# Kernel optimization log

Measured on AMD Instinct MI355X. Metric: run time of the kernel, lower is better.

## Reference

```python
import jax, jax.numpy as jnp
import numpy as np

VOCAB = 50000
EMB = 256
HID = 256
H = HID // 2          # per-direction LSTM hidden
NTAG = 14
START = 12
STOP = 13
SEQ = 8192
NEG = -10000.0


def setup_inputs() -> dict:
    key = jax.random.key(0)
    ks = jax.random.split(key, 14)
    s = 0.1
    sentence = jax.random.randint(ks[0], (SEQ,), 0, VOCAB)
    emb = jax.random.normal(ks[1], (VOCAB, EMB), jnp.float32) * s
    # PyTorch LSTM layout: gates stacked [i, f, g, o], shape [4H, in]
    wih_f = jax.random.normal(ks[2], (4 * H, EMB), jnp.float32) * s
    whh_f = jax.random.normal(ks[3], (4 * H, H), jnp.float32) * s
    bih_f = jax.random.normal(ks[4], (4 * H,), jnp.float32) * s
    bhh_f = jax.random.normal(ks[5], (4 * H,), jnp.float32) * s
    wih_b = jax.random.normal(ks[6], (4 * H, EMB), jnp.float32) * s
    whh_b = jax.random.normal(ks[7], (4 * H, H), jnp.float32) * s
    bih_b = jax.random.normal(ks[8], (4 * H,), jnp.float32) * s
    bhh_b = jax.random.normal(ks[9], (4 * H,), jnp.float32) * s
    w_tag = jax.random.normal(ks[10], (NTAG, HID), jnp.float32) * s
    b_tag = jax.random.normal(ks[11], (NTAG,), jnp.float32) * s
    transitions = jax.random.normal(ks[12], (NTAG, NTAG), jnp.float32)
    transitions = transitions.at[START, :].set(NEG).at[:, STOP].set(NEG)
    return {
        'sentence': sentence, 'emb': emb,
        'wih_f': wih_f, 'whh_f': whh_f, 'bih_f': bih_f, 'bhh_f': bhh_f,
        'wih_b': wih_b, 'whh_b': whh_b, 'bih_b': bih_b, 'bhh_b': bhh_b,
        'w_tag': w_tag, 'b_tag': b_tag, 'transitions': transitions,
    }


def _run_lstm(x, wih, whh, bih, bhh):
    # x: [L, EMB] -> hs: [L, H]; PyTorch gate order i, f, g, o
    def step(carry, xt):
        h, c = carry
        g = xt @ wih.T + h @ whh.T + bih + bhh
        i, f, gg, o = jnp.split(g, 4)
        i = jax.nn.sigmoid(i)
        f = jax.nn.sigmoid(f)
        gg = jnp.tanh(gg)
        o = jax.nn.sigmoid(o)
        c = f * c + i * gg
        h = o * jnp.tanh(c)
        return (h, c), h
    h0 = (jnp.zeros((H,), x.dtype), jnp.zeros((H,), x.dtype))
    _, hs = jax.lax.scan(step, h0, x)
    return hs


def _lstm_feats(sentence, emb, wih_f, whh_f, bih_f, bhh_f,
                wih_b, whh_b, bih_b, bhh_b, w_tag, b_tag):
    x = emb[sentence]                                   # [L, EMB]
    hf = _run_lstm(x, wih_f, whh_f, bih_f, bhh_f)       # [L, H]
    hb = _run_lstm(x[::-1], wih_b, whh_b, bih_b, bhh_b)[::-1]
    out = jnp.concatenate([hf, hb], axis=1)             # [L, HID]
    return out @ w_tag.T + b_tag                        # [L, NTAG]


def _viterbi(feats, transitions):
    init = jnp.full((NTAG,), NEG, feats.dtype).at[START].set(0.0)

    def step(fv, feat):
        scores = fv[None, :] + transitions   # [next_tag, prev_tag]
        bptr = jnp.argmax(scores, axis=1)    # best prev for each next
        fv_new = jnp.max(scores, axis=1) + feat
        return fv_new, bptr

    fv, bptrs = jax.lax.scan(step, init, feats)   # bptrs: [L, NTAG]
    terminal = fv + transitions[STOP]
    best = jnp.argmax(terminal)
    score = terminal[best]

    def back(tag, bptr_t):
        return bptr_t[tag], tag

    # reverse scan: emit tag at each position, walk backpointers to front
    _, path = jax.lax.scan(back, best, bptrs, reverse=True)  # [L]
    return score, path


def reference(sentence, emb, wih_f, whh_f, bih_f, bhh_f,
              wih_b, whh_b, bih_b, bhh_b, w_tag, b_tag, transitions):
    feats = _lstm_feats(sentence, emb, wih_f, whh_f, bih_f, bhh_f,
                        wih_b, whh_b, bih_b, bhh_b, w_tag, b_tag)
    return _viterbi(feats, transitions)
```

## Files before the change

### kernel.cpp

```cpp
#include <hip/hip_runtime.h>
#include <hip/hip_fp16.h>
#include <math.h>

#define SEQ    8192
#define EMBD   256
#define HD     128
#define GATES  512
#define NTAGS  14
#define TAG_START 12
#define TAG_STOP  13
#define NEGV   (-10000.0f)

static constexpr size_t OFF_X     = 0;
static constexpr size_t OFF_WT    = OFF_X + (size_t)SEQ * EMBD;
static constexpr size_t OFF_BSUM  = OFF_WT + (size_t)EMBD * 1024;
static constexpr size_t OFF_GF    = OFF_BSUM + 1024;
static constexpr size_t OFF_GB    = OFF_GF + (size_t)(SEQ + 4) * GATES;
static constexpr size_t OFF_HF    = OFF_GB + (size_t)(SEQ + 4) * GATES;
static constexpr size_t OFF_HB    = OFF_HF + (size_t)SEQ * HD;
static constexpr size_t OFF_FEATS = OFF_HB + (size_t)SEQ * HD;
static constexpr size_t OFF_BP    = OFF_FEATS + (size_t)(SEQ + 8) * 16;
static constexpr size_t OFF_AC    = OFF_BP + (size_t)SEQ * 16 / 4;
static constexpr size_t OFF_FVB   = OFF_AC + (size_t)64 * 256;
static constexpr size_t OFF_SB    = OFF_FVB + 1024;

#define LOG2E  1.4426950408889634f
#define LOG2E2 2.8853900817779268f

typedef _Float16 half2_t __attribute__((ext_vector_type(2)));

__device__ __forceinline__ float fast_rcp(float x) { return __builtin_amdgcn_rcpf(x); }
__device__ __forceinline__ float bcast_lane(float x, int lane) {
  return __int_as_float(__builtin_amdgcn_readlane(__float_as_int(x), lane));
}
__device__ __forceinline__ float max3f(float a, float b, float c) {
  return fmaxf(fmaxf(a, b), c);
}
__device__ __forceinline__ float max14(const float s[NTAGS]) {
  float m0 = max3f(s[0], s[1], s[2]);
  float m1 = max3f(s[3], s[4], s[5]);
  float m2 = max3f(s[6], s[7], s[8]);
  float m3 = max3f(s[9], s[10], s[11]);
  float m4 = fmaxf(s[12], s[13]);
  return max3f(max3f(m0, m1, m2), m3, m4);
}
template<int CTRL>
__device__ __forceinline__ float quad_dpp(float x) {
  int xi = __float_as_int(x);
  int r = __builtin_amdgcn_update_dpp(xi, xi, CTRL, 0xF, 0xF, false);
  return __int_as_float(r);
}

__device__ __forceinline__ float dot2acc(half2_t a, half2_t b, float c) {
#if __has_builtin(__builtin_amdgcn_fdot2)
  return __builtin_amdgcn_fdot2(a, b, c, false);
#else
  return fmaf((float)a[0], (float)b[0], fmaf((float)a[1], (float)b[1], c));
#endif
}

__device__ __forceinline__ float sigf(float x) {
  return fast_rcp(1.0f + exp2f(x * -LOG2E));
}
__device__ __forceinline__ float tanhf_(float x) {
  return fmaf(2.0f, fast_rcp(1.0f + exp2f(x * -LOG2E2)), -1.0f);
}

__device__ __forceinline__ void lds_barrier() {
  __builtin_amdgcn_sched_barrier(0);
  asm volatile("s_waitcnt lgkmcnt(0)" ::: "memory");
  __builtin_amdgcn_s_barrier();
  __builtin_amdgcn_sched_barrier(0);
}

__device__ __forceinline__ void argmax14(const float s[NTAGS], float& bv, int& bi) {
#define MRG(va, ia, vb, ib, vo, io) { bool c_ = (vb) > (va); (vo) = c_ ? (vb) : (va); (io) = c_ ? (ib) : (ia); }
  float v0, v1, v2, v3, v4, v5, v6; int i0, i1, i2, i3, i4, i5, i6;
  MRG(s[0], 0, s[1], 1, v0, i0); MRG(s[2], 2, s[3], 3, v1, i1);
  MRG(s[4], 4, s[5], 5, v2, i2); MRG(s[6], 6, s[7], 7, v3, i3);
  MRG(s[8], 8, s[9], 9, v4, i4); MRG(s[10], 10, s[11], 11, v5, i5);
  MRG(s[12], 12, s[13], 13, v6, i6);
  float w0, w1, w2; int j0, j1, j2;
  MRG(v0, i0, v1, i1, w0, j0); MRG(v2, i2, v3, i3, w1, j1); MRG(v4, i4, v5, i5, w2, j2);
  float x0, x1; int y0, y1;
  MRG(w0, j0, w1, j1, x0, y0); MRG(w2, j2, v6, i6, x1, y1);
  MRG(x0, y0, x1, y1, bv, bi);
#undef MRG
}

__global__ void prep_k(const float* __restrict__ wihf, const float* __restrict__ wihb,
                       const float* __restrict__ bihf, const float* __restrict__ bhhf,
                       const float* __restrict__ bihb, const float* __restrict__ bhhb,
                       float* __restrict__ WT, float* __restrict__ bsum) {
  if (blockIdx.x < 1024) {
    int e = blockIdx.x * 256 + threadIdx.x;
    int k = e >> 10, c = e & 1023;
    int cq = c & 511;
    int src = (cq & 3) * HD + (cq >> 2);
    WT[e] = (c < GATES) ? wihf[(size_t)src * EMBD + k] : wihb[(size_t)src * EMBD + k];
  } else {
    for (int i = 0; i < 4; ++i) {
      int c = threadIdx.x + i * 256;
      int cq = c & 511;
      int src = (cq & 3) * HD + (cq >> 2);
      bsum[c] = (c < GATES) ? (bihf[src] + bhhf[src]) : (bihb[src] + bhhb[src]);
    }
  }
}

__global__ void gather_k(const int* __restrict__ sent, const float* __restrict__ emb,
                         float* __restrict__ X) {
  int t = blockIdx.x;
  int row = sent[t];
  ((float4*)(X + (size_t)t * EMBD))[threadIdx.x] =
      ((const float4*)(emb + (size_t)row * EMBD))[threadIdx.x];
}

__global__ __launch_bounds__(256) void gemm_k(const float* __restrict__ X,
                                              const float* __restrict__ WT,
                                              const float* __restrict__ bsum,
                                              float* __restrict__ Gf, float* __restrict__ Gb) {
  __shared__ __align__(16) float As[32][68];
  __shared__ __align__(16) float Bs[32][64];
  const int tid = threadIdx.x;
  const int cb = blockIdx.x * 64;
  const int tb = blockIdx.y * 64;
  const bool flip = (cb >= GATES);
  const int ty = tid >> 4, tx = tid & 15;
  float acc[4][4] = {};

  const int r  = tid >> 2;
  const int kq = (tid & 3) * 8;
  const int kB = tid >> 3;
  const int n8 = (tid & 7) * 8;

  const int trow = tb + r;
  const int src = flip ? (SEQ - 1 - trow) : trow;

  for (int k0 = 0; k0 < EMBD; k0 += 32) {
    const float* xp = X + (size_t)src * EMBD + k0 + kq;
    float4 xa = *(const float4*)xp;
    float4 xb = *(const float4*)(xp + 4);
    As[kq + 0][r] = xa.x; As[kq + 1][r] = xa.y; As[kq + 2][r] = xa.z; As[kq + 3][r] = xa.w;
    As[kq + 4][r] = xb.x; As[kq + 5][r] = xb.y; As[kq + 6][r] = xb.z; As[kq + 7][r] = xb.w;
    const float* wp = WT + (size_t)(k0 + kB) * 1024 + cb + n8;
    *(float4*)&Bs[kB][n8]     = *(const float4*)wp;
    *(float4*)&Bs[kB][n8 + 4] = *(const float4*)(wp + 4);
    __syncthreads();
    #pragma unroll
    for (int k = 0; k < 32; ++k) {
      float4 av = *(const float4*)&As[k][ty * 4];
      float4 bv = *(const float4*)&Bs[k][tx * 4];
      acc[0][0] = fmaf(av.x, bv.x, acc[0][0]); acc[0][1] = fmaf(av.x, bv.y, acc[0][1]);
      acc[0][2] = fmaf(av.x, bv.z, acc[0][2]); acc[0][3] = fmaf(av.x, bv.w, acc[0][3]);
      acc[1][0] = fmaf(av.y, bv.x, acc[1][0]); acc[1][1] = fmaf(av.y, bv.y, acc[1][1]);
      acc[1][2] = fmaf(av.y, bv.z, acc[1][2]); acc[1][3] = fmaf(av.y, bv.w, acc[1][3]);
      acc[2][0] = fmaf(av.z, bv.x, acc[2][0]); acc[2][1] = fmaf(av.z, bv.y, acc[2][1]);
      acc[2][2] = fmaf(av.z, bv.z, acc[2][2]); acc[2][3] = fmaf(av.z, bv.w, acc[2][3]);
      acc[3][0] = fmaf(av.w, bv.x, acc[3][0]); acc[3][1] = fmaf(av.w, bv.y, acc[3][1]);
      acc[3][2] = fmaf(av.w, bv.z, acc[3][2]); acc[3][3] = fmaf(av.w, bv.w, acc[3][3]);
    }
    __syncthreads();
  }
  float4 bz = *(const float4*)&bsum[cb + tx * 4];
  #pragma unroll
  for (int mm = 0; mm < 4; ++mm) {
    int t = tb + ty * 4 + mm;
    float4 v = { acc[mm][0] + bz.x, acc[mm][1] + bz.y, acc[mm][2] + bz.z, acc[mm][3] + bz.w };
    if (!flip) *(float4*)&Gf[(size_t)t * GATES + cb + tx * 4] = v;
    else       *(float4*)&Gb[(size_t)t * GATES + (cb - GATES) + tx * 4] = v;
  }
}

__global__ __launch_bounds__(256, 1) void lstm_k(
    const float* __restrict__ whhf, const float* __restrict__ whhb,
    const float* __restrict__ Gf, const float* __restrict__ Gb,
    float* __restrict__ HF, float* __restrict__ HB) {
  const int dir = blockIdx.x;
  const float* __restrict__ G   = dir ? Gb : Gf;
  float* __restrict__ Hout      = dir ? HB : HF;
  const float* __restrict__ whh = dir ? whhb : whhf;
  const int tt = threadIdx.x;
  const int j = tt >> 1;
  const int s = tt & 1;
  const bool s0 = (s == 0);

  half2_t w2[4][32];
  #pragma unroll
  for (int gi = 0; gi < 4; ++gi) {
    const float* wr = whh + (size_t)(gi * HD + j) * HD + s * 64;
    #pragma unroll
    for (int kk = 0; kk < 32; ++kk) {
      half2_t w; w[0] = (_Float16)wr[2 * kk]; w[1] = (_Float16)wr[2 * kk + 1];
      w2[gi][kk] = w;
    }
  }

  __shared__ __align__(16) __half hA[HD], hB[HD];
  if (tt < HD) hA[tt] = __float2half_rn(0.0f);
  float cst = 0.0f;

  const float* gpA = G + 4 * j;
  const float* gpB = G + GATES + 4 * j;
  float4 gA = *(const float4*)gpA; gpA += 2 * GATES;
  float4 gB = *(const float4*)gpB; gpB += 2 * GATES;

  float* hout = Hout + (size_t)(dir ? (SEQ - 1) : 0) * HD + j;
  const ptrdiff_t hstep = dir ? -(ptrdiff_t)HD : (ptrdiff_t)HD;

  lds_barrier();

  auto step = [&](const __half* hrd, __half* hwr, float4& gslot, const float*& gptr) {
    float4 gcur = gslot;
    gslot = *(const float4*)gptr;
    gptr += 2 * GATES;

    const float4* hp = (const float4*)(hrd + (s << 6));
    float a[4][2] = {};
    #pragma unroll
    for (int i = 0; i < 8; ++i) {
      float4 hv = hp[i];
      const half2_t* hh = (const half2_t*)&hv;
      #pragma unroll
      for (int m = 0; m < 4; ++m) {
        const int kk = i * 4 + m;
        a[0][kk & 1] = dot2acc(w2[0][kk], hh[m], a[0][kk & 1]);
        a[1][kk & 1] = dot2acc(w2[1][kk], hh[m], a[1][kk & 1]);
        a[2][kk & 1] = dot2acc(w2[2][kk], hh[m], a[2][kk & 1]);
        a[3][kk & 1] = dot2acc(w2[3][kk], hh[m], a[3][kk & 1]);
      }
    }
    float p0 = a[0][0] + a[0][1];
    float p1 = a[1][0] + a[1][1];
    float p2 = a[2][0] + a[2][1];
    float p3 = a[3][0] + a[3][1];

    p0 += quad_dpp<0xB1>(p0);
    p1 += quad_dpp<0xB1>(p1);
    p2 += quad_dpp<0xB1>(p2);
    p3 += quad_dpp<0xB1>(p3);

    float i_ = sigf(p0 + gcur.x);
    float f_ = sigf(p1 + gcur.y);
    float g_ = tanhf_(p2 + gcur.z);
    float o_ = sigf(p3 + gcur.w);
    cst = fmaf(f_, cst, i_ * g_);
    float hj = o_ * tanhf_(cst);
    if (s0) { hwr[j] = __float2half_rn(hj); *hout = hj; }
    hout += hstep;
    lds_barrier();
  };

  for (int t = 0; t < SEQ; t += 2) {
    step(hA, hB, gA, gpA);
    step(hB, hA, gB, gpB);
  }
}

__global__ void feats_k(const float* __restrict__ HF, const float* __restrict__ HB,
                        const float* __restrict__ wtag, const float* __restrict__ btag,
                        float* __restrict__ feats) {
  const int t = blockIdx.x, l = threadIdx.x;
  float2 a = ((const float2*)(HF + (size_t)t * HD))[l];
  float2 b = ((const float2*)(HB + (size_t)t * HD))[l];
  float p[NTAGS];
  #pragma unroll
  for (int n = 0; n < NTAGS; ++n) {
    const float* wr = wtag + (size_t)n * 256;
    float2 w0 = ((const float2*)wr)[l];
    float2 w1 = ((const float2*)(wr + HD))[l];
    p[n] = a.x * w0.x + a.y * w0.y + b.x * w1.x + b.y * w1.y;
  }
  #pragma unroll
  for (int n = 0; n < NTAGS; ++n) {
    float v = p[n];
    for (int off = 32; off > 0; off >>= 1) v += __shfl_down(v, off);
    if (l == 0) feats[(size_t)t * 16 + n] = v + btag[n];
  }
}

__global__ __launch_bounds__(256) void vit_a(const float* __restrict__ feats,
                                             const float* __restrict__ trans,
                                             float* __restrict__ Ac) {
  const int c = blockIdx.x;
  const int tid = threadIdx.x;
  const int n = tid % NTAGS, p = tid / NTAGS;
  const bool act = tid < NTAGS * NTAGS;
  __shared__ __align__(16) float fl[128][16];
  __shared__ float Ab[2][NTAGS][17];

  const float4* fsrc = (const float4*)(feats + (size_t)c * 128 * 16);
  #pragma unroll
  for (int i = 0; i < 2; ++i)
    ((float4*)&fl[0][0])[tid + i * 256] = fsrc[tid + i * 256];

  float Tr[NTAGS];
  if (act) {
    #pragma unroll
    for (int qq = 0; qq < NTAGS; ++qq) Tr[qq] = trans[n * NTAGS + qq];
  }
  __syncthreads();
  if (act) Ab[0][n][p] = Tr[p] + fl[0][n];
  __syncthreads();

  int cur = 0;
  for (int tl = 1; tl < 128; ++tl) {
    if (act) {
      float s[NTAGS];
      #pragma unroll
      for (int qq = 0; qq < NTAGS; ++qq) s[qq] = Tr[qq] + Ab[cur][qq][p];
      Ab[cur ^ 1][n][p] = max14(s) + fl[tl][n];
    }
    __syncthreads();
    cur ^= 1;
  }
  if (act) Ac[(size_t)c * 256 + n * 16 + p] = Ab[cur][n][p];
}

__global__ void vit_b(const float* __restrict__ trans, const float* __restrict__ Ac,
                      float* __restrict__ fvb, float* __restrict__ out,
                      float* __restrict__ sb) {
  const int n = threadIdx.x;
  const bool act = n < NTAGS;
  float fv = (n == TAG_START) ? 0.0f : NEGV;
  for (int c = 0; c < 64; ++c) {
    if (act) fvb[c * 16 + n] = fv;
    float Ar[NTAGS];
    #pragma unroll
    for (int p = 0; p < NTAGS; ++p) Ar[p] = act ? Ac[(size_t)c * 256 + n * 16 + p] : NEGV;
    float s[NTAGS];
    #pragma unroll
    for (int p = 0; p < NTAGS; ++p) s[p] = Ar[p] + bcast_lane(fv, p);
    float nf = max14(s);
    fv = act ? nf : NEGV;
  }
  float tn = fv + (act ? trans[TAG_STOP * NTAGS + n] : NEGV);
  float tv[NTAGS];
  #pragma unroll
  for (int p = 0; p < NTAGS; ++p) tv[p] = bcast_lane(tn, p);
  if (n == 0) {
    float bv; int bi;
    argmax14(tv, bv, bi);
    out[0] = bv;
    ((int*)sb)[0] = bi;
  }
}

__global__ void vit_c(const float* __restrict__ feats, const float* __restrict__ trans,
                      const float* __restrict__ fvb, unsigned char* __restrict__ bpg) {
  const int c = blockIdx.x;
  const int n = threadIdx.x;
  const bool act = n < NTAGS;
  float Tn[NTAGS];
  #pragma unroll
  for (int p = 0; p < NTAGS; ++p) Tn[p] = act ? trans[n * NTAGS + p] : 0.0f;
  float fv = act ? fvb[c * 16 + n] : NEGV;
  const int t0 = c * 128;

  float fbuf[8];
  #pragma unroll
  for (int u = 0; u < 8; ++u) fbuf[u] = act ? feats[(size_t)(t0 + u) * 16 + n] : 0.0f;

  for (int tb = 0; tb < 128; tb += 8) {
    #pragma unroll
    for (int u = 0; u < 8; ++u) {
      const int t = t0 + tb + u;
      float ftc = fbuf[u];
      fbuf[u] = act ? feats[(size_t)(t + 8) * 16 + n] : 0.0f;
      float s[NTAGS];
      #pragma unroll
      for (int p = 0; p < NTAGS; ++p) s[p] = bcast_lane(fv, p) + Tn[p];
      float bv = max14(s);
      fv = bv + ftc;
      int bi = 13;
      #pragma unroll
      for (int p = 12; p >= 0; --p) bi = (s[p] == bv) ? p : bi;
      if (act) bpg[(size_t)t * 16 + n] = (unsigned char)bi;
    }
  }
}

__global__ __launch_bounds__(1024) void vit_d(const unsigned char* __restrict__ bpg,
                                              const float* __restrict__ sb,
                                              float* __restrict__ out) {
  __shared__ int sh_M[64 * 16];
  __shared__ int sh_B[64];
  const int tid = threadIdx.x;
  {
    const int c = tid >> 4, k = tid & 15;
    if (c >= 1 && c < 64 && k < NTAGS) {
      int x = k;
      for (int i = 127; i >= 0; --i) x = bpg[((size_t)(c * 128 + i)) * 16 + x];
      sh_M[c * 16 + k] = x;
    }
  }
  __syncthreads();
  if (tid == 0) {
    int b = ((const int*)sb)[0];
    sh_B[63] = b;
    for (int c = 63; c >= 1; --c) { b = sh_M[c * 16 + b]; sh_B[c - 1] = b; }
  }
  __syncthreads();
  if (tid < 64) {
    const int c = tid;
    int x = sh_B[c];
    out[1 + c * 128 + 127] = (float)x;
    for (int i = 127; i >= 1; --i) {
      x = bpg[((size_t)(c * 128 + i)) * 16 + x];
      out[1 + c * 128 + i - 1] = (float)x;
    }
  }
}

extern "C" void kernel_launch(void* const* d_in, const int* in_sizes, int n_in,
                              void* d_out, int out_size, void* d_ws, size_t ws_size,
                              hipStream_t stream) {
  (void)in_sizes; (void)n_in; (void)out_size; (void)ws_size;
  const int*   sent = (const int*)d_in[0];
  const float* emb  = (const float*)d_in[1];
  const float* wihf = (const float*)d_in[2];
  const float* whhf = (const float*)d_in[3];
  const float* bihf = (const float*)d_in[4];
  const float* bhhf = (const float*)d_in[5];
  const float* wihb = (const float*)d_in[6];
  const float* whhb = (const float*)d_in[7];
  const float* bihb = (const float*)d_in[8];
  const float* bhhb = (const float*)d_in[9];
  const float* wtag = (const float*)d_in[10];
  const float* btag = (const float*)d_in[11];
  const float* trans = (const float*)d_in[12];

  float* ws = (float*)d_ws;
  float* X    = ws + OFF_X;
  float* WT   = ws + OFF_WT;
  float* BS   = ws + OFF_BSUM;
  float* Gf   = ws + OFF_GF;
  float* Gb   = ws + OFF_GB;
  float* HF   = ws + OFF_HF;
  float* HB   = ws + OFF_HB;
  float* FE   = ws + OFF_FEATS;
  unsigned char* bpg = (unsigned char*)(ws + OFF_BP);
  float* AC   = ws + OFF_AC;
  float* FVB  = ws + OFF_FVB;
  float* SB   = ws + OFF_SB;
  float* out = (float*)d_out;

  prep_k<<<1025, 256, 0, stream>>>(wihf, wihb, bihf, bhhf, bihb, bhhb, WT, BS);
  gather_k<<<SEQ, 64, 0, stream>>>(sent, emb, X);
  gemm_k<<<dim3(16, 128), 256, 0, stream>>>(X, WT, BS, Gf, Gb);
  lstm_k<<<2, 256, 0, stream>>>(whhf, whhb, Gf, Gb, HF, HB);
  feats_k<<<SEQ, 64, 0, stream>>>(HF, HB, wtag, btag, FE);
  vit_a<<<64, 256, 0, stream>>>(FE, trans, AC);
  vit_b<<<1, 64, 0, stream>>>(trans, AC, FVB, out, SB);
  vit_c<<<64, 64, 0, stream>>>(FE, trans, FVB, bpg);
  vit_d<<<1, 1024, 0, stream>>>(bpg, SB, out);
}
```

Baseline: 4.740 ms.

## Run forward and backward LSTM directions interleaved in one workgroup

The two LSTM directions, previously two independent workgroups, now run in a single 256-thread workgroup that advances both recurrences in the same step. Each thread keeps both directions' recurrent weights in registers, and the two independent dot-product chains interleave so their latencies hide each other. Only one barrier per step is needed for both directions. The cost is twice the register footprint, which risks spills, and all the work is serialized onto one compute unit instead of two running in parallel.

```diff
diff --git a/kernel.cpp b/kernel.cpp
--- a/kernel.cpp
+++ b/kernel.cpp
@@ -176,84 +176,104 @@
     const float* __restrict__ whhf, const float* __restrict__ whhb,
     const float* __restrict__ Gf, const float* __restrict__ Gb,
     float* __restrict__ HF, float* __restrict__ HB) {
-  const int dir = blockIdx.x;
-  const float* __restrict__ G   = dir ? Gb : Gf;
-  float* __restrict__ Hout      = dir ? HB : HF;
-  const float* __restrict__ whh = dir ? whhb : whhf;
   const int tt = threadIdx.x;
   const int j = tt >> 1;
   const int s = tt & 1;
   const bool s0 = (s == 0);
 
-  half2_t w2[4][32];
+  half2_t wf[4][32], wb[4][32];
   #pragma unroll
   for (int gi = 0; gi < 4; ++gi) {
-    const float* wr = whh + (size_t)(gi * HD + j) * HD + s * 64;
+    const float* wrf = whhf + (size_t)(gi * HD + j) * HD + s * 64;
+    const float* wrb = whhb + (size_t)(gi * HD + j) * HD + s * 64;
     #pragma unroll
     for (int kk = 0; kk < 32; ++kk) {
-      half2_t w; w[0] = (_Float16)wr[2 * kk]; w[1] = (_Float16)wr[2 * kk + 1];
-      w2[gi][kk] = w;
-    }
-  }
-
-  __shared__ __align__(16) __half hA[HD], hB[HD];
-  if (tt < HD) hA[tt] = __float2half_rn(0.0f);
-  float cst = 0.0f;
-
-  const float* gpA = G + 4 * j;
-  const float* gpB = G + GATES + 4 * j;
-  float4 gA = *(const float4*)gpA; gpA += 2 * GATES;
-  float4 gB = *(const float4*)gpB; gpB += 2 * GATES;
-
-  float* hout = Hout + (size_t)(dir ? (SEQ - 1) : 0) * HD + j;
-  const ptrdiff_t hstep = dir ? -(ptrdiff_t)HD : (ptrdiff_t)HD;
+      half2_t w; w[0] = (_Float16)wrf[2 * kk]; w[1] = (_Float16)wrf[2 * kk + 1];
+      wf[gi][kk] = w;
+      half2_t v; v[0] = (_Float16)wrb[2 * kk]; v[1] = (_Float16)wrb[2 * kk + 1];
+      wb[gi][kk] = v;
+    }
+  }
+
+  __shared__ __align__(16) __half hAf[HD], hBf[HD], hAb[HD], hBb[HD];
+  if (tt < HD) { hAf[tt] = __float2half_rn(0.0f); hAb[tt] = __float2half_rn(0.0f); }
+  float cf = 0.0f, cbw = 0.0f;
+
+  const float* gpAf = Gf + 4 * j;
+  const float* gpBf = Gf + GATES + 4 * j;
+  const float* gpAb = Gb + 4 * j;
+  const float* gpBb = Gb + GATES + 4 * j;
+  float4 gAf = *(const float4*)gpAf; gpAf += 2 * GATES;
+  float4 gBf = *(const float4*)gpBf; gpBf += 2 * GATES;
+  float4 gAb = *(const float4*)gpAb; gpAb += 2 * GATES;
+  float4 gBb = *(const float4*)gpBb; gpBb += 2 * GATES;
+
+  float* houtf = HF + j;
+  float* houtb = HB + (size_t)(SEQ - 1) * HD + j;
+  const int hoff = s << 6;
 
   lds_barrier();
 
-  auto step = [&](const __half* hrd, __half* hwr, float4& gslot, const float*& gptr) {
-    float4 gcur = gslot;
-    gslot = *(const float4*)gptr;
-    gptr += 2 * GATES;
-
-    const float4* hp = (const float4*)(hrd + (s << 6));
-    float a[4][2] = {};
+  auto step = [&](const __half* hrdF, __half* hwrF, float4& gsF, const float*& gpF,
+                  const __half* hrdB, __half* hwrB, float4& gsB, const float*& gpB) {
+    float4 gcf = gsF; gsF = *(const float4*)gpF; gpF += 2 * GATES;
+    float4 gcb = gsB; gsB = *(const float4*)gpB; gpB += 2 * GATES;
+
+    const float4* hpf = (const float4*)(hrdF + hoff);
+    const float4* hpb = (const float4*)(hrdB + hoff);
+    float af[4][2] = {}, ab[4][2] = {};
     #pragma unroll
     for (int i = 0; i < 8; ++i) {
-      float4 hv = hp[i];
-      const half2_t* hh = (const half2_t*)&hv;
+      float4 hvf = hpf[i];
+      float4 hvb = hpb[i];
+      const half2_t* hf2 = (const half2_t*)&hvf;
+      const half2_t* hb2 = (const half2_t*)&hvb;
       #pragma unroll
       for (int m = 0; m < 4; ++m) {
         const int kk = i * 4 + m;
-        a[0][kk & 1] = dot2acc(w2[0][kk], hh[m], a[0][kk & 1]);
-        a[1][kk & 1] = dot2acc(w2[1][kk], hh[m], a[1][kk & 1]);
-        a[2][kk & 1] = dot2acc(w2[2][kk], hh[m], a[2][kk & 1]);
-        a[3][kk & 1] = dot2acc(w2[3][kk], hh[m], a[3][kk & 1]);
+        af[0][kk & 1] = dot2acc(wf[0][kk], hf2[m], af[0][kk & 1]);
+        af[1][kk & 1] = dot2acc(wf[1][kk], hf2[m], af[1][kk & 1]);
+        af[2][kk & 1] = dot2acc(wf[2][kk], hf2[m], af[2][kk & 1]);
+        af[3][kk & 1] = dot2acc(wf[3][kk], hf2[m], af[3][kk & 1]);
+        ab[0][kk & 1] = dot2acc(wb[0][kk], hb2[m], ab[0][kk & 1]);
+        ab[1][kk & 1] = dot2acc(wb[1][kk], hb2[m], ab[1][kk & 1]);
+        ab[2][kk & 1] = dot2acc(wb[2][kk], hb2[m], ab[2][kk & 1]);
+        ab[3][kk & 1] = dot2acc(wb[3][kk], hb2[m], ab[3][kk & 1]);
       }
     }
-    float p0 = a[0][0] + a[0][1];
-    float p1 = a[1][0] + a[1][1];
-    float p2 = a[2][0] + a[2][1];
-    float p3 = a[3][0] + a[3][1];
-
-    p0 += quad_dpp<0xB1>(p0);
-    p1 += quad_dpp<0xB1>(p1);
-    p2 += quad_dpp<0xB1>(p2);
-    p3 += quad_dpp<0xB1>(p3);
-
-    float i_ = sigf(p0 + gcur.x);
-    float f_ = sigf(p1 + gcur.y);
-    float g_ = tanhf_(p2 + gcur.z);
-    float o_ = sigf(p3 + gcur.w);
-    cst = fmaf(f_, cst, i_ * g_);
-    float hj = o_ * tanhf_(cst);
-    if (s0) { hwr[j] = __float2half_rn(hj); *hout = hj; }
-    hout += hstep;
+    float pf0 = af[0][0] + af[0][1], pf1 = af[1][0] + af[1][1];
+    float pf2 = af[2][0] + af[2][1], pf3 = af[3][0] + af[3][1];
+    float pb0 = ab[0][0] + ab[0][1], pb1 = ab[1][0] + ab[1][1];
+    float pb2 = ab[2][0] + ab[2][1], pb3 = ab[3][0] + ab[3][1];
+
+    pf0 += quad_dpp<0xB1>(pf0); pf1 += quad_dpp<0xB1>(pf1);
+    pf2 += quad_dpp<0xB1>(pf2); pf3 += quad_dpp<0xB1>(pf3);
+    pb0 += quad_dpp<0xB1>(pb0); pb1 += quad_dpp<0xB1>(pb1);
+    pb2 += quad_dpp<0xB1>(pb2); pb3 += quad_dpp<0xB1>(pb3);
+
+    float if_ = sigf(pf0 + gcf.x);
+    float ib_ = sigf(pb0 + gcb.x);
+    float ff_ = sigf(pf1 + gcf.y);
+    float fb_ = sigf(pb1 + gcb.y);
+    float gf_ = tanhf_(pf2 + gcf.z);
+    float gb_ = tanhf_(pb2 + gcb.z);
+    float of_ = sigf(pf3 + gcf.w);
+    float ob_ = sigf(pb3 + gcb.w);
+    cf  = fmaf(ff_, cf,  if_ * gf_);
+    cbw = fmaf(fb_, cbw, ib_ * gb_);
+    float hjf = of_ * tanhf_(cf);
+    float hjb = ob_ * tanhf_(cbw);
+    if (s0) {
+      hwrF[j] = __float2half_rn(hjf); *houtf = hjf;
+      hwrB[j] = __float2half_rn(hjb); *houtb = hjb;
+    }
+    houtf += HD; houtb -= HD;
     lds_barrier();
   };
 
   for (int t = 0; t < SEQ; t += 2) {
-    step(hA, hB, gA, gpA);
-    step(hB, hA, gB, gpB);
+    step(hAf, hBf, gAf, gpAf, hAb, hBb, gAb, gpAb);
+    step(hBf, hAf, gBf, gpBf, hBb, hAb, gBb, gpBb);
   }
 }
 
@@ -448,7 +468,7 @@
   prep_k<<<1025, 256, 0, stream>>>(wihf, wihb, bihf, bhhf, bihb, bhhb, WT, BS);
   gather_k<<<SEQ, 64, 0, stream>>>(sent, emb, X);
   gemm_k<<<dim3(16, 128), 256, 0, stream>>>(X, WT, BS, Gf, Gb);
-  lstm_k<<<2, 256, 0, stream>>>(whhf, whhb, Gf, Gb, HF, HB);
+  lstm_k<<<1, 256, 0, stream>>>(whhf, whhb, Gf, Gb, HF, HB);
   feats_k<<<SEQ, 64, 0, stream>>>(HF, HB, wtag, btag, FE);
   vit_a<<<64, 256, 0, stream>>>(FE, trans, AC);
   vit_b<<<1, 64, 0, stream>>>(trans, AC, FVB, out, SB);
```

Result: slower. 12.31 ms (+159.8%).
